# Optimization experiments

Measured on AMD Instinct MI355X. Metric: run time of the kernel, lower is better.

The kernel has to match this reference:

```python
import jax, jax.numpy as jnp
import numpy as np
import math

COND_DIM = 64
HIDDEN = 128
NUM_SIN = 2
SQRT2 = 1.4142135623730951


def fused_leaky_relu(x, bias):
    # stylegan2 fused bias + leaky relu (slope 0.2) with sqrt(2) gain
    return jax.nn.leaky_relu(x + bias, negative_slope=0.2) * SQRT2


def equal_linear2(x, W, b, lr_mul=1.0, activation=False):
    scale = lr_mul / math.sqrt(W.shape[1])
    out = x @ (W * scale).T
    if activation:
        return fused_leaky_relu(out, b * lr_mul)
    return out + b * lr_mul


def coords_to_sinusoidals(x, num_sinusoidals=NUM_SIN, multiplier=2.0):
    # x: [P, 1] -> [P, 2*num_sinusoidals], freq_type='mult': freqs = multiplier**i
    freqs = multiplier ** jnp.arange(num_sinusoidals, dtype=x.dtype)  # [S]
    ang = x * freqs  # [P, S]
    return jnp.concatenate([jnp.sin(ang), jnp.cos(ang)], axis=-1)


def setup_inputs() -> dict:
    key = jax.random.key(0)
    ks = jax.random.split(key, 10)
    B, N = 64, 8192
    coord_in = 2 * NUM_SIN  # 4
    in1 = coord_in + COND_DIM  # 68
    in2 = HIDDEN + COND_DIM    # 192
    coords = jax.random.normal(ks[0], (B, N, 2), dtype=jnp.float32)
    c = jax.random.normal(ks[1], (B, N, COND_DIM), dtype=jnp.float32)
    # EqualLinear2 weights init uniform(-1,1)/lr_mul; last layer zero in torch,
    # use small random values here so gradients/outputs are non-trivial.
    Wx1 = jax.random.uniform(ks[2], (HIDDEN, in1), minval=-1.0, maxval=1.0)
    bx1 = jnp.zeros((HIDDEN,), jnp.float32)
    Wx2 = jax.random.uniform(ks[3], (2, in2), minval=-1.0, maxval=1.0) * 0.1
    bx2 = jnp.zeros((2,), jnp.float32)
    Wy1 = jax.random.uniform(ks[4], (HIDDEN, in1), minval=-1.0, maxval=1.0)
    by1 = jnp.zeros((HIDDEN,), jnp.float32)
    Wy2 = jax.random.uniform(ks[5], (2, in2), minval=-1.0, maxval=1.0) * 0.1
    by2 = jnp.zeros((2,), jnp.float32)
    return {"coords": coords, "c": c,
            "Wx1": Wx1, "bx1": bx1, "Wx2": Wx2, "bx2": bx2,
            "Wy1": Wy1, "by1": by1, "Wy2": Wy2, "by2": by2}


def reference(coords, c, Wx1, bx1, Wx2, bx2, Wy1, by1, Wy2, by2):
    initial_shape = coords.shape[:-1]
    coords2 = coords.reshape(-1, coords.shape[-1])  # [P, 2]
    cf = c.reshape(-1, c.shape[-1])                 # [P, cond]
    x = coords2[:, 0:1]
    y = coords2[:, 1:2]

    # x branch -> affine params for y
    h = coords_to_sinusoidals(x / 10.0)
    h = equal_linear2(jnp.concatenate([h, cf], -1), Wx1, bx1, activation=True)
    o = equal_linear2(jnp.concatenate([h, cf], -1), Wx2, bx2, activation=False)
    y_log_scale = jnp.clip(o[:, 0:1], -5.0, 5.0)
    y_bias = o[:, 1:2]
    y = y * jnp.exp(y_log_scale) + y_bias

    # y branch -> affine params for x
    h = coords_to_sinusoidals(y / 10.0)
    h = equal_linear2(jnp.concatenate([h, cf], -1), Wy1, by1, activation=True)
    o = equal_linear2(jnp.concatenate([h, cf], -1), Wy2, by2, activation=False)
    x_log_scale = jnp.clip(o[:, 0:1], -5.0, 5.0)
    x_bias = o[:, 1:2]
    x = x * jnp.exp(x_log_scale) + x_bias

    warped = jnp.concatenate([x, y], -1).reshape(*initial_shape, -1)
    log_jac = jnp.concatenate([x_log_scale + y_log_scale], -1)
    log_jac = (x_log_scale + y_log_scale).reshape(*initial_shape, -1)
    return warped, log_jac
```

## Files before the change

### kernel.cpp

```cpp
#include <hip/hip_runtime.h>

typedef unsigned short u16t;
typedef short short8 __attribute__((ext_vector_type(8)));
typedef float f32x4 __attribute__((ext_vector_type(4)));

__device__ __forceinline__ u16t f2bf_rne(float f) {
  unsigned u = __builtin_bit_cast(unsigned, f);
  u += 0x7FFFu + ((u >> 16) & 1u);
  return (u16t)(u >> 16);
}
__device__ __forceinline__ unsigned pk2(float a, float b) {
  unsigned ua = __builtin_bit_cast(unsigned, a) + 0x8000u;
  unsigned ub = __builtin_bit_cast(unsigned, b) + 0x8000u;
  return (ua >> 16) | (ub & 0xFFFF0000u);
}
union S8U { short8 s; unsigned w[4]; };
__device__ __forceinline__ short8 pack8f(float4 a, float4 b) {
  S8U u;
  u.w[0] = pk2(a.x, a.y); u.w[1] = pk2(a.z, a.w);
  u.w[2] = pk2(b.x, b.y); u.w[3] = pk2(b.z, b.w);
  return u.s;
}

#define WS_WB  0
#define WS_BS  32768
#define WS_FF  49152
#define WS_BC  65536

__global__ void prep_kernel(const float* __restrict__ Wx1, const float* __restrict__ bx1,
                            const float* __restrict__ Wx2,
                            const float* __restrict__ Wy1, const float* __restrict__ by1,
                            const float* __restrict__ Wy2,
                            char* __restrict__ ws)
{
  const int tid = threadIdx.x;
  const int p = tid >> 9, nt = (tid >> 6) & 7, lane = tid & 63;
  const int l15 = lane & 15, quad = lane >> 4;
  const float* W1 = p ? Wy1 : Wx1;
  const float* B1 = p ? by1 : bx1;
  const float* W2 = p ? Wy2 : Wx2;
  const int n = nt * 16 + l15;
  const float* rp = W1 + n * 68;
  short8 bb0, bb1, bs = (short8)0;
  #pragma unroll
  for (int j = 0; j < 8; ++j) {
    bb0[j] = (short)f2bf_rne(rp[4 + quad * 8 + j]);
    bb1[j] = (short)f2bf_rne(rp[36 + quad * 8 + j]);
  }
  if (quad == 0) {
    #pragma unroll
    for (int j = 0; j < 4; ++j) bs[j] = (short)f2bf_rne(rp[j]);
  }
  short8* wb = (short8*)(ws + WS_WB);
  wb[((p * 8 + nt) * 2 + 0) * 64 + lane] = bb0;
  wb[((p * 8 + nt) * 2 + 1) * 64 + lane] = bb1;
  ((short8*)(ws + WS_BS))[(p * 8 + nt) * 64 + lane] = bs;
  const float SQ2 = 1.41421356237309515f;
  float4 ff;
  ff.x = B1[n]; ff.y = W2[n] * SQ2; ff.z = W2[192 + n] * SQ2; ff.w = 0.f;
  ((float4*)(ws + WS_FF))[(p * 8 + nt) * 64 + lane] = ff;

  if (tid < 256) {
    const int p2 = tid >> 7, h = (tid >> 6) & 1, ln = tid & 63;
    const int l2 = ln & 15, q2 = ln >> 4;
    const float* W2b = p2 ? Wy2 : Wx2;
    short8 bc = (short8)0;
    if (l2 < 2) {
      #pragma unroll
      for (int j = 0; j < 8; ++j)
        bc[j] = (short)f2bf_rne(W2b[l2 * 192 + 128 + h * 32 + q2 * 8 + j]);
    }
    ((short8*)(ws + WS_BC))[(p2 * 2 + h) * 64 + ln] = bc;
  }
}

__global__ __launch_bounds__(256, 4)
void icb_main(const float* __restrict__ g_coords, const float* __restrict__ g_c,
              const float* __restrict__ g_bx2, const float* __restrict__ g_by2,
              const char* __restrict__ ws, float* __restrict__ g_out)
{
  const int tid  = threadIdx.x;
  const int lane = tid & 63, wave = tid >> 6;
  const int l15  = lane & 15, quad = lane >> 4;
  const int wbase = blockIdx.x * 128 + wave * 32;

  const short8* wb  = (const short8*)(ws + WS_WB);
  const short8* wbs = (const short8*)(ws + WS_BS);
  const float4* wf  = (const float4*)(ws + WS_FF);
  const short8* wbc = (const short8*)(ws + WS_BC);

  short8 aC0[2], aC1[2];
  float xold[2], yold[2];
  #pragma unroll
  for (int mt = 0; mt < 2; ++mt) {
    const int r = wbase + mt * 16 + l15;
    const float4* cr = (const float4*)(g_c + (size_t)r * 64);
    float4 a0 = cr[quad * 2],     a1 = cr[quad * 2 + 1];
    float4 a2 = cr[8 + quad * 2], a3 = cr[8 + quad * 2 + 1];
    aC0[mt] = pack8f(a0, a1);
    aC1[mt] = pack8f(a2, a3);
    float2 p = ((const float2*)g_coords)[r];
    xold[mt] = p.x; yold[mt] = p.y;
  }

  const float s1 = 0.121267812518166f;
  const float s2 = 0.0721687836487032f;

  float vin[2], xnew[2], ynew[2], xls[2], yls[2];
  vin[0] = xold[0]; vin[1] = xold[1];

  #pragma unroll 1
  for (int path = 0; path < 2; ++path) {
    const int pb = path * 8;
    const float* b2 = path ? g_by2 : g_bx2;
    const float b20 = b2[0], b21 = b2[1];

    short8 aS[2];
    #pragma unroll
    for (int mt = 0; mt < 2; ++mt) {
      short8 f = (short8)0;
      if (quad == 0) {
        float a = vin[mt] * 0.1f;
        float sa, ca;
        __sincosf(a, &sa, &ca);
        float s2a = 2.0f * sa * ca;
        float c2a = 1.0f - 2.0f * sa * sa;
        f[0] = (short)f2bf_rne(sa); f[1] = (short)f2bf_rne(s2a);
        f[2] = (short)f2bf_rne(ca); f[3] = (short)f2bf_rne(c2a);
      }
      aS[mt] = f;
    }

    short8 bc0 = wbc[(path * 2 + 0) * 64 + lane];
    short8 bc1 = wbc[(path * 2 + 1) * 64 + lane];
    f32x4 acc8[2];
    #pragma unroll
    for (int mt = 0; mt < 2; ++mt) {
      f32x4 a = {0.f, 0.f, 0.f, 0.f};
      a = __builtin_amdgcn_mfma_f32_16x16x32_bf16(aC0[mt], bc0, a, 0, 0, 0);
      a = __builtin_amdgcn_mfma_f32_16x16x32_bf16(aC1[mt], bc1, a, 0, 0, 0);
      acc8[mt] = a;
    }

    float hp[2][4][2];
    #pragma unroll
    for (int mt = 0; mt < 2; ++mt)
      #pragma unroll
      for (int j = 0; j < 4; ++j) { hp[mt][j][0] = 0.f; hp[mt][j][1] = 0.f; }

    #pragma unroll 2
    for (int nt = 0; nt < 8; ++nt) {
      short8 bb0 = wb[((pb + nt) * 2 + 0) * 64 + lane];
      short8 bb1 = wb[((pb + nt) * 2 + 1) * 64 + lane];
      short8 bs  = wbs[(pb + nt) * 64 + lane];
      float4 ff  = wf[(pb + nt) * 64 + lane];
      #pragma unroll
      for (int mt = 0; mt < 2; ++mt) {
        f32x4 acc = {0.f, 0.f, 0.f, 0.f};
        acc = __builtin_amdgcn_mfma_f32_16x16x32_bf16(aC0[mt], bb0, acc, 0, 0, 0);
        acc = __builtin_amdgcn_mfma_f32_16x16x32_bf16(aC1[mt], bb1, acc, 0, 0, 0);
        acc = __builtin_amdgcn_mfma_f32_16x16x32_bf16(aS[mt],  bs,  acc, 0, 0, 0);
        #pragma unroll
        for (int j = 0; j < 4; ++j) {
          float v = fmaf(s1, acc[j], ff.x);
          float h = fmaxf(v, 0.2f * v);
          hp[mt][j][0] = fmaf(h, ff.y, hp[mt][j][0]);
          hp[mt][j][1] = fmaf(h, ff.z, hp[mt][j][1]);
        }
      }
    }

    #pragma unroll
    for (int mt = 0; mt < 2; ++mt)
      #pragma unroll
      for (int j = 0; j < 4; ++j) {
        hp[mt][j][0] += (l15 == 0) ? acc8[mt][j] : 0.f;
        hp[mt][j][1] += (l15 == 1) ? acc8[mt][j] : 0.f;
      }

    #pragma unroll
    for (int mt = 0; mt < 2; ++mt)
      #pragma unroll
      for (int j = 0; j < 4; ++j)
        #pragma unroll
        for (int o = 0; o < 2; ++o) {
          float v = hp[mt][j][o];
          v += __shfl_xor(v, 1);
          v += __shfl_xor(v, 2);
          v += __shfl_xor(v, 4);
          v += __shfl_xor(v, 8);
          hp[mt][j][o] = v;
        }

    const int jm = l15 & 3;
    const int src = ((l15 >> 2) << 4) | jm;
    #pragma unroll
    for (int mt = 0; mt < 2; ++mt) {
      float t0[4], t1[4];
      #pragma unroll
      for (int j = 0; j < 4; ++j) {
        t0[j] = fmaf(s2, hp[mt][j][0], b20);
        t1[j] = fmaf(s2, hp[mt][j][1], b21);
      }
      float s0 = (jm & 1) ? t0[1] : t0[0], s0b = (jm & 1) ? t0[3] : t0[2];
      s0 = (jm & 2) ? s0b : s0;
      float s1v = (jm & 1) ? t1[1] : t1[0], s1b = (jm & 1) ? t1[3] : t1[2];
      s1v = (jm & 2) ? s1b : s1v;
      float lsraw = __shfl(s0, src);
      float brow  = __shfl(s1v, src);

      float ls = fminf(fmaxf(lsraw, -5.f), 5.f);
      float e  = __expf(ls);
      if (path == 0) {
        yls[mt]  = ls;
        ynew[mt] = fmaf(yold[mt], e, brow);
        vin[mt]  = ynew[mt];
      } else {
        xls[mt]  = ls;
        xnew[mt] = fmaf(xold[mt], e, brow);
      }
    }
  }

  if (lane < 16) {
    #pragma unroll
    for (int mt = 0; mt < 2; ++mt) {
      int R = wbase + mt * 16 + lane;
      float2 pw; pw.x = xnew[mt]; pw.y = ynew[mt];
      reinterpret_cast<float2*>(g_out)[R] = pw;
      g_out[1048576 + R] = xls[mt] + yls[mt];
    }
  }
}

extern "C" void kernel_launch(void* const* d_in, const int* in_sizes, int n_in,
                              void* d_out, int out_size, void* d_ws, size_t ws_size,
                              hipStream_t stream) {
  (void)in_sizes; (void)n_in; (void)out_size; (void)ws_size;
  prep_kernel<<<1, 1024, 0, stream>>>(
      (const float*)d_in[2], (const float*)d_in[3], (const float*)d_in[4],
      (const float*)d_in[6], (const float*)d_in[7], (const float*)d_in[8],
      (char*)d_ws);
  icb_main<<<4096, 256, 0, stream>>>(
      (const float*)d_in[0], (const float*)d_in[1],
      (const float*)d_in[5], (const float*)d_in[9],
      (const char*)d_ws, (float*)d_out);
}
```

Before: 241.2 us.

## Stage compacted weight tables in LDS with larger blocks

The prep kernel now writes compacted tables: the sinusoid weights as packed uint2 and the bias/second-layer factors as 16-entry float4 rows instead of per-lane replicas. This shrinks the workspace to about 43KB. The main kernel now runs 1024-thread blocks that copy this table into shared memory once per block, overlapping the copy with the loads of c. All inner-loop weight reads then come from LDS instead of global/L1. The cost is a block-wide barrier, heavy LDS use per block and a much tighter register budget from the new launch bounds, which could cause spills.

```diff
diff --git a/kernel.cpp b/kernel.cpp
--- a/kernel.cpp
+++ b/kernel.cpp
@@ -24,8 +24,9 @@
 
 #define WS_WB  0
 #define WS_BS  32768
-#define WS_FF  49152
-#define WS_BC  65536
+#define WS_FF  34816
+#define WS_BC  38912
+#define WS_BYTES 43008
 
 __global__ void prep_kernel(const float* __restrict__ Wx1, const float* __restrict__ bx1,
                             const float* __restrict__ Wx2,
@@ -33,75 +34,100 @@
                             const float* __restrict__ Wy2,
                             char* __restrict__ ws)
 {
-  const int tid = threadIdx.x;
-  const int p = tid >> 9, nt = (tid >> 6) & 7, lane = tid & 63;
+  const int b = blockIdx.x;
+  const int lane = threadIdx.x;
+  const int p = b >> 3, nt = b & 7;
   const int l15 = lane & 15, quad = lane >> 4;
   const float* W1 = p ? Wy1 : Wx1;
   const float* B1 = p ? by1 : bx1;
   const float* W2 = p ? Wy2 : Wx2;
   const int n = nt * 16 + l15;
   const float* rp = W1 + n * 68;
-  short8 bb0, bb1, bs = (short8)0;
+  short8 bb0, bb1;
   #pragma unroll
   for (int j = 0; j < 8; ++j) {
     bb0[j] = (short)f2bf_rne(rp[4 + quad * 8 + j]);
     bb1[j] = (short)f2bf_rne(rp[36 + quad * 8 + j]);
   }
-  if (quad == 0) {
-    #pragma unroll
-    for (int j = 0; j < 4; ++j) bs[j] = (short)f2bf_rne(rp[j]);
-  }
   short8* wb = (short8*)(ws + WS_WB);
   wb[((p * 8 + nt) * 2 + 0) * 64 + lane] = bb0;
   wb[((p * 8 + nt) * 2 + 1) * 64 + lane] = bb1;
-  ((short8*)(ws + WS_BS))[(p * 8 + nt) * 64 + lane] = bs;
-  const float SQ2 = 1.41421356237309515f;
-  float4 ff;
-  ff.x = B1[n]; ff.y = W2[n] * SQ2; ff.z = W2[192 + n] * SQ2; ff.w = 0.f;
-  ((float4*)(ws + WS_FF))[(p * 8 + nt) * 64 + lane] = ff;
-
-  if (tid < 256) {
-    const int p2 = tid >> 7, h = (tid >> 6) & 1, ln = tid & 63;
-    const int l2 = ln & 15, q2 = ln >> 4;
+
+  if (quad == 0) {
+    uint2 t;
+    t.x = (unsigned)f2bf_rne(rp[0]) | ((unsigned)f2bf_rne(rp[1]) << 16);
+    t.y = (unsigned)f2bf_rne(rp[2]) | ((unsigned)f2bf_rne(rp[3]) << 16);
+    ((uint2*)(ws + WS_BS))[(p * 8 + nt) * 16 + l15] = t;
+  }
+
+  if (lane < 16) {
+    const float SQ2 = 1.41421356237309515f;
+    const int nn = nt * 16 + lane;
+    float4 ff;
+    ff.x = B1[nn]; ff.y = W2[nn] * SQ2; ff.z = W2[192 + nn] * SQ2; ff.w = 0.f;
+    ((float4*)(ws + WS_FF))[(p * 8 + nt) * 16 + lane] = ff;
+  }
+
+  if (b < 4) {
+    const int p2 = b >> 1, h = b & 1;
     const float* W2b = p2 ? Wy2 : Wx2;
     short8 bc = (short8)0;
-    if (l2 < 2) {
+    if (l15 < 2) {
       #pragma unroll
       for (int j = 0; j < 8; ++j)
-        bc[j] = (short)f2bf_rne(W2b[l2 * 192 + 128 + h * 32 + q2 * 8 + j]);
-    }
-    ((short8*)(ws + WS_BC))[(p2 * 2 + h) * 64 + ln] = bc;
-  }
-}
-
-__global__ __launch_bounds__(256, 4)
+        bc[j] = (short)f2bf_rne(W2b[l15 * 192 + 128 + h * 32 + quad * 8 + j]);
+    }
+    ((short8*)(ws + WS_BC))[(p2 * 2 + h) * 64 + lane] = bc;
+  }
+}
+
+__global__ __launch_bounds__(1024, 8)
 void icb_main(const float* __restrict__ g_coords, const float* __restrict__ g_c,
               const float* __restrict__ g_bx2, const float* __restrict__ g_by2,
               const char* __restrict__ ws, float* __restrict__ g_out)
 {
+  __shared__ float4 s_tab4[WS_BYTES / 16];
+  char* s_tab = (char*)s_tab4;
+
   const int tid  = threadIdx.x;
   const int lane = tid & 63, wave = tid >> 6;
   const int l15  = lane & 15, quad = lane >> 4;
-  const int wbase = blockIdx.x * 128 + wave * 32;
-
-  const short8* wb  = (const short8*)(ws + WS_WB);
-  const short8* wbs = (const short8*)(ws + WS_BS);
-  const float4* wf  = (const float4*)(ws + WS_FF);
-  const short8* wbc = (const short8*)(ws + WS_BC);
+  const int wbase = blockIdx.x * 512 + wave * 32;
+
+  float4 ra[2][4]; float2 rco[2];
+  #pragma unroll
+  for (int mt = 0; mt < 2; ++mt) {
+    const int r = wbase + mt * 16 + l15;
+    const float4* cr = (const float4*)(g_c + (size_t)r * 64);
+    ra[mt][0] = cr[quad * 2];     ra[mt][1] = cr[quad * 2 + 1];
+    ra[mt][2] = cr[8 + quad * 2]; ra[mt][3] = cr[8 + quad * 2 + 1];
+    rco[mt] = ((const float2*)g_coords)[r];
+  }
+
+  {
+    const float4* src = (const float4*)ws;
+    #pragma unroll
+    for (int k = 0; k < 3; ++k) {
+      const int t = tid + k * 1024;
+      if (t < WS_BYTES / 16) s_tab4[t] = src[t];
+    }
+  }
 
   short8 aC0[2], aC1[2];
   float xold[2], yold[2];
   #pragma unroll
   for (int mt = 0; mt < 2; ++mt) {
-    const int r = wbase + mt * 16 + l15;
-    const float4* cr = (const float4*)(g_c + (size_t)r * 64);
-    float4 a0 = cr[quad * 2],     a1 = cr[quad * 2 + 1];
-    float4 a2 = cr[8 + quad * 2], a3 = cr[8 + quad * 2 + 1];
-    aC0[mt] = pack8f(a0, a1);
-    aC1[mt] = pack8f(a2, a3);
-    float2 p = ((const float2*)g_coords)[r];
-    xold[mt] = p.x; yold[mt] = p.y;
-  }
+    aC0[mt] = pack8f(ra[mt][0], ra[mt][1]);
+    aC1[mt] = pack8f(ra[mt][2], ra[mt][3]);
+    xold[mt] = rco[mt].x; yold[mt] = rco[mt].y;
+  }
+
+  __syncthreads();
+
+  const short8* wb  = (const short8*)(s_tab + WS_WB);
+  const uint2*  wbs = (const uint2*) (s_tab + WS_BS);
+  const float4* wf  = (const float4*)(s_tab + WS_FF);
+  const short8* wbc = (const short8*)(s_tab + WS_BC);
 
   const float s1 = 0.121267812518166f;
   const float s2 = 0.0721687836487032f;
@@ -152,8 +178,10 @@
     for (int nt = 0; nt < 8; ++nt) {
       short8 bb0 = wb[((pb + nt) * 2 + 0) * 64 + lane];
       short8 bb1 = wb[((pb + nt) * 2 + 1) * 64 + lane];
-      short8 bs  = wbs[(pb + nt) * 64 + lane];
-      float4 ff  = wf[(pb + nt) * 64 + lane];
+      uint2  bsv = wbs[(pb + nt) * 16 + l15];
+      S8U su; su.w[0] = bsv.x; su.w[1] = bsv.y; su.w[2] = bsv.x; su.w[3] = bsv.y;
+      const short8 bs = su.s;
+      float4 ff  = wf[(pb + nt) * 16 + l15];
       #pragma unroll
       for (int mt = 0; mt < 2; ++mt) {
         f32x4 acc = {0.f, 0.f, 0.f, 0.f};
@@ -237,11 +265,11 @@
                               void* d_out, int out_size, void* d_ws, size_t ws_size,
                               hipStream_t stream) {
   (void)in_sizes; (void)n_in; (void)out_size; (void)ws_size;
-  prep_kernel<<<1, 1024, 0, stream>>>(
+  prep_kernel<<<16, 64, 0, stream>>>(
       (const float*)d_in[2], (const float*)d_in[3], (const float*)d_in[4],
       (const float*)d_in[6], (const float*)d_in[7], (const float*)d_in[8],
       (char*)d_ws);
-  icb_main<<<4096, 256, 0, stream>>>(
+  icb_main<<<1024, 1024, 0, stream>>>(
       (const float*)d_in[0], (const float*)d_in[1],
       (const float*)d_in[5], (const float*)d_in[9],
       (const char*)d_ws, (float*)d_out);
```

Result: slower. 449.3 us (+86.3%).
